# Kernel tuning notes

Hardware: AMD Instinct MI355X
Metric: run time of the kernel (lower is better)

The kernel has to match this reference:

```python
import jax, jax.numpy as jnp
from jax import lax
import numpy as np

EPS = 1e-12  # matches torch F.normalize eps


def _dtw_similarity(s1, s2):
    # s1: [L1, D], s2: [L2, D]
    L1, L2 = s1.shape[0], s2.shape[0]
    s1n = s1 / jnp.maximum(jnp.linalg.norm(s1, axis=1, keepdims=True), EPS)
    s2n = s2 / jnp.maximum(jnp.linalg.norm(s2, axis=1, keepdims=True), EPS)
    dist = 1.0 - s1n @ s2n.T  # [L1, L2] cosine distance

    # DTW DP. Row 0 is a cumsum; each subsequent row has a left-to-right
    # sequential dependency handled by an inner scan.
    row0 = jnp.cumsum(dist[0])

    def row_step(prev_row, d_row):
        # prev_row: dtw[i-1, :], d_row: dist[i, :]
        first = prev_row[0] + d_row[0]  # dtw[i, 0]
        # min(prev[j], prev[j-1]) for j >= 1 (vectorized part of the min)
        p = jnp.minimum(prev_row[1:], prev_row[:-1])

        def col_step(c, inp):
            dj, pj = inp
            new = dj + jnp.minimum(pj, c)  # c = dtw[i, j-1]
            return new, new

        _, rest = lax.scan(col_step, first, (d_row[1:], p))
        new_row = jnp.concatenate([first[None], rest])
        return new_row, None

    last_row, _ = lax.scan(row_step, row0, dist[1:])
    dtw_distance = last_row[-1]
    normalized = dtw_distance / (L1 + L2)
    return 1.0 / (1.0 + normalized)


def setup_inputs() -> dict:
    key = jax.random.key(0)
    k1, k2 = jax.random.split(key)
    seq1 = jax.random.normal(k1, (16, 1024, 768), dtype=jnp.float32)
    seq2 = jax.random.normal(k2, (16, 1024, 768), dtype=jnp.float32)
    return {"seq1": seq1, "seq2": seq2}


def reference(seq1, seq2):
    # seq1: [B, L1, D], seq2: [B, L2, D] -> [B]
    return jax.vmap(_dtw_similarity)(seq1, seq2)
```

## Files before the change

kernel.cpp:

```cpp
#include <hip/hip_runtime.h>
#include <hip/hip_bf16.h>

typedef __attribute__((ext_vector_type(4))) float f32x4;
typedef __attribute__((ext_vector_type(8))) short bf16x8;

#define DINF 1e30f

__device__ __forceinline__ unsigned short f2bf(float f) {
    unsigned int u = __builtin_bit_cast(unsigned int, f);
    u += 0x7FFFu + ((u >> 16) & 1u);
    return (unsigned short)(u >> 16);
}

__global__ __launch_bounds__(256) void zero_holes_kernel(float4* __restrict__ skew) {
    const int idx = blockIdx.x;
    const int bt  = idx / 127;
    const int pr  = idx % 127;
    const int h   = pr * 2 + (threadIdx.x >> 7);
    const int row = h < 126 ? h : 1024 + (h - 126);
    const int c   = threadIdx.x & 127;
    skew[((size_t)bt * 1152 + row) * 128 + c] = (float4){0.f, 0.f, 0.f, 0.f};
}

__global__ __launch_bounds__(256) void norm_bf16_kernel(
    const float* __restrict__ s1, const float* __restrict__ s2,
    __hip_bfloat16* __restrict__ o1, __hip_bfloat16* __restrict__ o2) {
    const int gb = blockIdx.x;
    const float* in;
    __hip_bfloat16* out;
    int rowbase;
    if (gb < 4096) { in = s1; out = o1; rowbase = gb * 4; }
    else           { in = s2; out = o2; rowbase = (gb - 4096) * 4; }
    const int wv = threadIdx.x >> 6;
    const int l  = threadIdx.x & 63;
    const int row = rowbase + wv;

    const float* rp = in + (size_t)row * 768 + l * 4;
    float4 x0 = *(const float4*)(rp);
    float4 x1 = *(const float4*)(rp + 256);
    float4 x2 = *(const float4*)(rp + 512);

    float s = x0.x*x0.x + x0.y*x0.y + x0.z*x0.z + x0.w*x0.w
            + x1.x*x1.x + x1.y*x1.y + x1.z*x1.z + x1.w*x1.w
            + x2.x*x2.x + x2.y*x2.y + x2.z*x2.z + x2.w*x2.w;
#pragma unroll
    for (int off = 32; off > 0; off >>= 1) s += __shfl_xor(s, off, 64);

    const float inv = 1.0f / fmaxf(sqrtf(s), 1e-12f);

    __hip_bfloat16* op = out + (size_t)row * 768 + l * 4;
    ushort4 o;
    o.x = f2bf(x0.x*inv); o.y = f2bf(x0.y*inv); o.z = f2bf(x0.z*inv); o.w = f2bf(x0.w*inv);
    *(ushort4*)(op) = o;
    o.x = f2bf(x1.x*inv); o.y = f2bf(x1.y*inv); o.z = f2bf(x1.z*inv); o.w = f2bf(x1.w*inv);
    *(ushort4*)(op + 256) = o;
    o.x = f2bf(x2.x*inv); o.y = f2bf(x2.y*inv); o.z = f2bf(x2.z*inv); o.w = f2bf(x2.w*inv);
    *(ushort4*)(op + 512) = o;
}

#define GLOAD_LDS16(g, l)                                                      \
    __builtin_amdgcn_global_load_lds(                                          \
        (const __attribute__((address_space(1))) void*)(g),                    \
        (__attribute__((address_space(3))) void*)(l), 16, 0, 0)

__global__ __launch_bounds__(256) void gemm_dist_kernel(
    const __hip_bfloat16* __restrict__ A, const __hip_bfloat16* __restrict__ B,
    __hip_bfloat16* __restrict__ skew) {
    __shared__ __hip_bfloat16 lA[128 * 64];
    __shared__ __hip_bfloat16 lB[128 * 64];

    const int blk  = (blockIdx.x & 7) * 128 + (blockIdx.x >> 3);
    const int b    = blk >> 6;
    const int tile = blk & 63;
    const int tm = tile >> 3, tn = tile & 7;
    const int tid  = threadIdx.x;
    const int lane = tid & 63, w = tid >> 6;
    const int lr = lane & 15, lg = lane >> 4;
    const int wm = w >> 1, wn = w & 1;

    const __hip_bfloat16* Ab = A + (size_t)b * (1024 * 768) + (size_t)(tm * 128) * 768;
    const __hip_bfloat16* Bb = B + (size_t)b * (1024 * 768) + (size_t)(tn * 128) * 768;

    const int srow = tid >> 3;
    const int scol = (tid & 7) * 8;

    char* lAb = (char*)lA;
    char* lBb = (char*)lB;

    f32x4 acc[4][4];
#pragma unroll
    for (int m = 0; m < 4; ++m)
#pragma unroll
        for (int n = 0; n < 4; ++n) acc[m][n] = (f32x4){0.f, 0.f, 0.f, 0.f};

    for (int k0 = 0; k0 < 768; k0 += 64) {
#pragma unroll
        for (int q = 0; q < 4; ++q) {
            GLOAD_LDS16(Ab + (size_t)(q * 32 + srow) * 768 + k0 + scol,
                        lAb + q * 4096 + w * 1024);
            GLOAD_LDS16(Bb + (size_t)(q * 32 + srow) * 768 + k0 + scol,
                        lBb + q * 4096 + w * 1024);
        }
        __syncthreads();

#pragma unroll
        for (int ks = 0; ks < 64; ks += 32) {
            bf16x8 af[4], bfr[4];
#pragma unroll
            for (int m = 0; m < 4; ++m)
                af[m] = *(const bf16x8*)&lA[(wm * 64 + m * 16 + lr) * 64 + ks + lg * 8];
#pragma unroll
            for (int n = 0; n < 4; ++n)
                bfr[n] = *(const bf16x8*)&lB[(wn * 64 + n * 16 + lr) * 64 + ks + lg * 8];
#pragma unroll
            for (int m = 0; m < 4; ++m)
#pragma unroll
                for (int n = 0; n < 4; ++n)
                    acc[m][n] = __builtin_amdgcn_mfma_f32_16x16x32_bf16(af[m], bfr[n], acc[m][n], 0, 0, 0);
        }
        __syncthreads();
    }

    unsigned short* S = (unsigned short*)skew + (size_t)b * (1152 * 1024);
#pragma unroll
    for (int m = 0; m < 4; ++m)
#pragma unroll
        for (int n = 0; n < 4; ++n) {
            const int cb = tn * 128 + wn * 64 + n * 16;
            const int soff = 2 * (cb >> 4);
#pragma unroll
            for (int r = 0; r < 4; ++r) {
                const int row = tm * 128 + wm * 64 + m * 16 + lg * 4 + r;
                S[(size_t)(row + soff) * 1024 + cb + lr] = f2bf(1.0f - acc[m][n][r]);
            }
        }
}


#define VWAIT(n) asm volatile("s_waitcnt vmcnt(" #n ")" ::: "memory")

#define GLDMA16(g, l)                                                          \
    __builtin_amdgcn_global_load_lds(                                          \
        (const __attribute__((address_space(1))) void*)(g),                    \
        (__attribute__((address_space(3))) void*)(l), 16, 0, 0)

#define LOADR(BK, SL, RW) do {                                                 \
    const char* g_ = Sb + ((size_t)(RW) << 11);                                \
    GLDMA16(g_,      &ring[BK][SL][0][0]);                                     \
    GLDMA16(g_ + 16, &ring[BK][SL][1][0]);                                     \
} while (0)

#define ISSUE8(BK, BASE) do {                                                  \
    LOADR(BK, 0, (BASE));     LOADR(BK, 1, (BASE) + 1);                        \
    LOADR(BK, 2, (BASE) + 2); LOADR(BK, 3, (BASE) + 3);                        \
    LOADR(BK, 4, (BASE) + 4); LOADR(BK, 5, (BASE) + 5);                        \
    LOADR(BK, 6, (BASE) + 6); LOADR(BK, 7, (BASE) + 7);                        \
} while (0)

#define DECLR(N) float4 N##_0, N##_1

#define DSRD(BK, SL, N) do {                                                   \
    N##_0 = ring[BK][SL][0][t]; N##_1 = ring[BK][SL][1][t];                    \
} while (0)

#define DSRD8(BK) do {                                                         \
    DSRD(BK, 0, R0); DSRD(BK, 1, R1); DSRD(BK, 2, R2); DSRD(BK, 3, R3);        \
    DSRD(BK, 4, R4); DSRD(BK, 5, R5); DSRD(BK, 6, R6); DSRD(BK, 7, R7);        \
} while (0)

#define STEPBODY(P, E0EXPR) do {                                               \
    unsigned u0_ = __builtin_bit_cast(unsigned, P##_0.x);                      \
    unsigned u1_ = __builtin_bit_cast(unsigned, P##_0.y);                      \
    unsigned u2_ = __builtin_bit_cast(unsigned, P##_0.z);                      \
    unsigned u3_ = __builtin_bit_cast(unsigned, P##_0.w);                      \
    unsigned u4_ = __builtin_bit_cast(unsigned, P##_1.x);                      \
    unsigned u5_ = __builtin_bit_cast(unsigned, P##_1.y);                      \
    unsigned u6_ = __builtin_bit_cast(unsigned, P##_1.z);                      \
    unsigned u7_ = __builtin_bit_cast(unsigned, P##_1.w);                      \
    float d0_  = __builtin_bit_cast(float, u0_ << 16);                         \
    float d1_  = __builtin_bit_cast(float, u0_ & 0xffff0000u);                 \
    float d2_  = __builtin_bit_cast(float, u1_ << 16);                         \
    float d3_  = __builtin_bit_cast(float, u1_ & 0xffff0000u);                 \
    float d4_  = __builtin_bit_cast(float, u2_ << 16);                         \
    float d5_  = __builtin_bit_cast(float, u2_ & 0xffff0000u);                 \
    float d6_  = __builtin_bit_cast(float, u3_ << 16);                         \
    float d7_  = __builtin_bit_cast(float, u3_ & 0xffff0000u);                 \
    float d8_  = __builtin_bit_cast(float, u4_ << 16);                         \
    float d9_  = __builtin_bit_cast(float, u4_ & 0xffff0000u);                 \
    float d10_ = __builtin_bit_cast(float, u5_ << 16);                         \
    float d11_ = __builtin_bit_cast(float, u5_ & 0xffff0000u);                 \
    float d12_ = __builtin_bit_cast(float, u6_ << 16);                         \
    float d13_ = __builtin_bit_cast(float, u6_ & 0xffff0000u);                 \
    float d14_ = __builtin_bit_cast(float, u7_ << 16);                         \
    float d15_ = __builtin_bit_cast(float, u7_ & 0xffff0000u);                 \
    float e0_ = (E0EXPR);                                                      \
    float c0_  = d0_  + e0_;                                                   \
    float c1_  = d1_  + fminf(fminf(p1,  p0),  c0_);                           \
    float c2_  = d2_  + fminf(fminf(p2,  p1),  c1_);                           \
    float c3_  = d3_  + fminf(fminf(p3,  p2),  c2_);                           \
    float c4_  = d4_  + fminf(fminf(p4,  p3),  c3_);                           \
    float c5_  = d5_  + fminf(fminf(p5,  p4),  c4_);                           \
    float c6_  = d6_  + fminf(fminf(p6,  p5),  c5_);                           \
    float c7_  = d7_  + fminf(fminf(p7,  p6),  c6_);                           \
    float c8_  = d8_  + fminf(fminf(p8,  p7),  c7_);                           \
    float c9_  = d9_  + fminf(fminf(p9,  p8),  c8_);                           \
    float c10_ = d10_ + fminf(fminf(p10, p9),  c9_);                           \
    float c11_ = d11_ + fminf(fminf(p11, p10), c10_);                          \
    float c12_ = d12_ + fminf(fminf(p12, p11), c11_);                          \
    float c13_ = d13_ + fminf(fminf(p13, p12), c12_);                          \
    float c14_ = d14_ + fminf(fminf(p14, p13), c13_);                          \
    float c15_ = d15_ + fminf(fminf(p15, p14), c14_);                          \
    p0=c0_; p1=c1_; p2=c2_; p3=c3_; p4=c4_; p5=c5_; p6=c6_; p7=c7_;            \
    p8=c8_; p9=c9_; p10=c10_; p11=c11_; p12=c12_; p13=c13_; p14=c14_; p15=c15_;\
    a3 = a2; a2 = a1;                                                          \
    a1 = __shfl_up(c15_, 1, 64);                                               \
    a1 = lane0 ? DINF : a1;                                                    \
} while (0)

#define STEPB(P)       STEPBODY(P, fminf(fminf(p0, a3), a2))
#define STEPB_FIRST(P) STEPBODY(P, lane0 ? 0.0f : fminf(fminf(p0, a3), a2))

#define STEP8() do {                                                           \
    STEPB(R0); STEPB(R1); STEPB(R2); STEPB(R3);                                \
    STEPB(R4); STEPB(R5); STEPB(R6); STEPB(R7);                                \
} while (0)

__global__ __launch_bounds__(64, 1) void dtw_dp_kernel(
    const __hip_bfloat16* __restrict__ skew, float* __restrict__ out) {
    __shared__ float4 ring[3][8][2][64];

    const int b = blockIdx.x;
    const int t = threadIdx.x;
    const bool lane0 = (t == 0);
    const char* Sb = (const char*)(skew + (size_t)b * (1152 * 1024)) + (t << 5);

    float p0 = DINF, p1 = DINF, p2 = DINF, p3 = DINF,
          p4 = DINF, p5 = DINF, p6 = DINF, p7 = DINF,
          p8 = DINF, p9 = DINF, p10 = DINF, p11 = DINF,
          p12 = DINF, p13 = DINF, p14 = DINF, p15 = DINF;
    float a1 = DINF, a2 = DINF, a3 = DINF;

    DECLR(R0); DECLR(R1); DECLR(R2); DECLR(R3);
    DECLR(R4); DECLR(R5); DECLR(R6); DECLR(R7);

    ISSUE8(0, 0);
    ISSUE8(1, 8);

    ISSUE8(2, 16);
    VWAIT(16);
    DSRD8(0);
    STEPB_FIRST(R0);
    STEPB(R1); STEPB(R2); STEPB(R3); STEPB(R4); STEPB(R5); STEPB(R6); STEPB(R7);

    int rb = 1, ib = 0, base = 24;
#pragma unroll 1
    for (int j = 1; j < 142; ++j) {
        ISSUE8(ib, base);
        VWAIT(16);
        DSRD8(rb);
        STEP8();
        rb = rb == 2 ? 0 : rb + 1;
        ib = ib == 2 ? 0 : ib + 1;
        base += 8;
    }

    VWAIT(8);
    DSRD8(1);
    STEP8();
    VWAIT(0);
    DSRD(2, 0, R0); DSRD(2, 1, R1); DSRD(2, 2, R2);
    DSRD(2, 3, R3); DSRD(2, 4, R4); DSRD(2, 5, R5);
    STEPB(R0); STEPB(R1); STEPB(R2); STEPB(R3); STEPB(R4); STEPB(R5);

    if (t == 63) out[b] = 1.0f / (1.0f + p15 * (1.0f / 2048.0f));
}

extern "C" void kernel_launch(void* const* d_in, const int* in_sizes, int n_in,
                              void* d_out, int out_size, void* d_ws, size_t ws_size,
                              hipStream_t stream) {
    const float* s1 = (const float*)d_in[0];
    const float* s2 = (const float*)d_in[1];
    float* out = (float*)d_out;

    char* ws = (char*)d_ws;
    __hip_bfloat16* Abf  = (__hip_bfloat16*)(ws);
    __hip_bfloat16* Bbf  = (__hip_bfloat16*)(ws + 25165824);
    __hip_bfloat16* skew = (__hip_bfloat16*)(ws + 50331648);

    zero_holes_kernel<<<16 * 127, 256, 0, stream>>>((float4*)skew);
    norm_bf16_kernel<<<8192, 256, 0, stream>>>(s1, s2, Abf, Bbf);
    gemm_dist_kernel<<<16 * 64, 256, 0, stream>>>(Abf, Bbf, skew);
    dtw_dp_kernel<<<16, 64, 0, stream>>>(skew, out);
}
```

Before: 260.8 us.

## Interleave two batch DTW chains per wavefront and pipeline LDS reads

```diff
diff --git a/kernel.cpp b/kernel.cpp
--- a/kernel.cpp
+++ b/kernel.cpp
@@ -144,135 +144,179 @@
         (const __attribute__((address_space(1))) void*)(g),                    \
         (__attribute__((address_space(3))) void*)(l), 16, 0, 0)
 
-#define LOADR(BK, SL, RW) do {                                                 \
-    const char* g_ = Sb + ((size_t)(RW) << 11);                                \
-    GLDMA16(g_,      &ring[BK][SL][0][0]);                                     \
-    GLDMA16(g_ + 16, &ring[BK][SL][1][0]);                                     \
+#define LOADR(BAT, BK, SL, RW) do {                                            \
+    const char* g_ = Sb##BAT + ((size_t)(RW) << 11);                           \
+    GLDMA16(g_,      &ring[BAT][BK][SL][0][0]);                                \
+    GLDMA16(g_ + 16, &ring[BAT][BK][SL][1][0]);                                \
 } while (0)
 
-#define ISSUE8(BK, BASE) do {                                                  \
-    LOADR(BK, 0, (BASE));     LOADR(BK, 1, (BASE) + 1);                        \
-    LOADR(BK, 2, (BASE) + 2); LOADR(BK, 3, (BASE) + 3);                        \
-    LOADR(BK, 4, (BASE) + 4); LOADR(BK, 5, (BASE) + 5);                        \
-    LOADR(BK, 6, (BASE) + 6); LOADR(BK, 7, (BASE) + 7);                        \
+#define ISSUE16(BK, BASE) do {                                                 \
+    LOADR(0, BK, 0, (BASE));     LOADR(1, BK, 0, (BASE));                      \
+    LOADR(0, BK, 1, (BASE) + 1); LOADR(1, BK, 1, (BASE) + 1);                  \
+    LOADR(0, BK, 2, (BASE) + 2); LOADR(1, BK, 2, (BASE) + 2);                  \
+    LOADR(0, BK, 3, (BASE) + 3); LOADR(1, BK, 3, (BASE) + 3);                  \
+    LOADR(0, BK, 4, (BASE) + 4); LOADR(1, BK, 4, (BASE) + 4);                  \
+    LOADR(0, BK, 5, (BASE) + 5); LOADR(1, BK, 5, (BASE) + 5);                  \
+    LOADR(0, BK, 6, (BASE) + 6); LOADR(1, BK, 6, (BASE) + 6);                  \
+    LOADR(0, BK, 7, (BASE) + 7); LOADR(1, BK, 7, (BASE) + 7);                  \
 } while (0)
 
-#define DECLR(N) float4 N##_0, N##_1
-
-#define DSRD(BK, SL, N) do {                                                   \
-    N##_0 = ring[BK][SL][0][t]; N##_1 = ring[BK][SL][1][t];                    \
+#define DSRD2(BK, SL, PA, PB) do {                                             \
+    PA##_0 = ring[0][BK][SL][0][t]; PB##_0 = ring[1][BK][SL][0][t];            \
+    PA##_1 = ring[0][BK][SL][1][t]; PB##_1 = ring[1][BK][SL][1][t];            \
 } while (0)
 
-#define DSRD8(BK) do {                                                         \
-    DSRD(BK, 0, R0); DSRD(BK, 1, R1); DSRD(BK, 2, R2); DSRD(BK, 3, R3);        \
-    DSRD(BK, 4, R4); DSRD(BK, 5, R5); DSRD(BK, 6, R6); DSRD(BK, 7, R7);        \
+#define BFLO(u) __builtin_bit_cast(float, (unsigned)((u) << 16))
+#define BFHI(u) __builtin_bit_cast(float, (unsigned)((u) & 0xffff0000u))
+
+#define STEPDUO(PA, PB, E0A, E0B) do {                                         \
+    unsigned uA0_ = __builtin_bit_cast(unsigned, PA##_0.x);                    \
+    unsigned uB0_ = __builtin_bit_cast(unsigned, PB##_0.x);                    \
+    unsigned uA1_ = __builtin_bit_cast(unsigned, PA##_0.y);                    \
+    unsigned uB1_ = __builtin_bit_cast(unsigned, PB##_0.y);                    \
+    unsigned uA2_ = __builtin_bit_cast(unsigned, PA##_0.z);                    \
+    unsigned uB2_ = __builtin_bit_cast(unsigned, PB##_0.z);                    \
+    unsigned uA3_ = __builtin_bit_cast(unsigned, PA##_0.w);                    \
+    unsigned uB3_ = __builtin_bit_cast(unsigned, PB##_0.w);                    \
+    unsigned uA4_ = __builtin_bit_cast(unsigned, PA##_1.x);                    \
+    unsigned uB4_ = __builtin_bit_cast(unsigned, PB##_1.x);                    \
+    unsigned uA5_ = __builtin_bit_cast(unsigned, PA##_1.y);                    \
+    unsigned uB5_ = __builtin_bit_cast(unsigned, PB##_1.y);                    \
+    unsigned uA6_ = __builtin_bit_cast(unsigned, PA##_1.z);                    \
+    unsigned uB6_ = __builtin_bit_cast(unsigned, PB##_1.z);                    \
+    unsigned uA7_ = __builtin_bit_cast(unsigned, PA##_1.w);                    \
+    unsigned uB7_ = __builtin_bit_cast(unsigned, PB##_1.w);                    \
+    float eA_ = (E0A);                  float eB_ = (E0B);                     \
+    float cA0_  = BFLO(uA0_) + eA_;                                            \
+    float cB0_  = BFLO(uB0_) + eB_;                                            \
+    float cA1_  = BFHI(uA0_) + fminf(fminf(pA1,  pA0),  cA0_);                 \
+    float cB1_  = BFHI(uB0_) + fminf(fminf(pB1,  pB0),  cB0_);                 \
+    float cA2_  = BFLO(uA1_) + fminf(fminf(pA2,  pA1),  cA1_);                 \
+    float cB2_  = BFLO(uB1_) + fminf(fminf(pB2,  pB1),  cB1_);                 \
+    float cA3_  = BFHI(uA1_) + fminf(fminf(pA3,  pA2),  cA2_);                 \
+    float cB3_  = BFHI(uB1_) + fminf(fminf(pB3,  pB2),  cB2_);                 \
+    float cA4_  = BFLO(uA2_) + fminf(fminf(pA4,  pA3),  cA3_);                 \
+    float cB4_  = BFLO(uB2_) + fminf(fminf(pB4,  pB3),  cB3_);                 \
+    float cA5_  = BFHI(uA2_) + fminf(fminf(pA5,  pA4),  cA4_);                 \
+    float cB5_  = BFHI(uB2_) + fminf(fminf(pB5,  pB4),  cB4_);                 \
+    float cA6_  = BFLO(uA3_) + fminf(fminf(pA6,  pA5),  cA5_);                 \
+    float cB6_  = BFLO(uB3_) + fminf(fminf(pB6,  pB5),  cB5_);                 \
+    float cA7_  = BFHI(uA3_) + fminf(fminf(pA7,  pA6),  cA6_);                 \
+    float cB7_  = BFHI(uB3_) + fminf(fminf(pB7,  pB6),  cB6_);                 \
+    float cA8_  = BFLO(uA4_) + fminf(fminf(pA8,  pA7),  cA7_);                 \
+    float cB8_  = BFLO(uB4_) + fminf(fminf(pB8,  pB7),  cB7_);                 \
+    float cA9_  = BFHI(uA4_) + fminf(fminf(pA9,  pA8),  cA8_);                 \
+    float cB9_  = BFHI(uB4_) + fminf(fminf(pB9,  pB8),  cB8_);                 \
+    float cA10_ = BFLO(uA5_) + fminf(fminf(pA10, pA9),  cA9_);                 \
+    float cB10_ = BFLO(uB5_) + fminf(fminf(pB10, pB9),  cB9_);                 \
+    float cA11_ = BFHI(uA5_) + fminf(fminf(pA11, pA10), cA10_);                \
+    float cB11_ = BFHI(uB5_) + fminf(fminf(pB11, pB10), cB10_);                \
+    float cA12_ = BFLO(uA6_) + fminf(fminf(pA12, pA11), cA11_);                \
+    float cB12_ = BFLO(uB6_) + fminf(fminf(pB12, pB11), cB11_);                \
+    float cA13_ = BFHI(uA6_) + fminf(fminf(pA13, pA12), cA12_);                \
+    float cB13_ = BFHI(uB6_) + fminf(fminf(pB13, pB12), cB12_);                \
+    float cA14_ = BFLO(uA7_) + fminf(fminf(pA14, pA13), cA13_);                \
+    float cB14_ = BFLO(uB7_) + fminf(fminf(pB14, pB13), cB13_);                \
+    float cA15_ = BFHI(uA7_) + fminf(fminf(pA15, pA14), cA14_);                \
+    float cB15_ = BFHI(uB7_) + fminf(fminf(pB15, pB14), cB14_);                \
+    pA0=cA0_; pA1=cA1_; pA2=cA2_; pA3=cA3_; pA4=cA4_; pA5=cA5_; pA6=cA6_;      \
+    pA7=cA7_; pA8=cA8_; pA9=cA9_; pA10=cA10_; pA11=cA11_; pA12=cA12_;          \
+    pA13=cA13_; pA14=cA14_; pA15=cA15_;                                        \
+    pB0=cB0_; pB1=cB1_; pB2=cB2_; pB3=cB3_; pB4=cB4_; pB5=cB5_; pB6=cB6_;      \
+    pB7=cB7_; pB8=cB8_; pB9=cB9_; pB10=cB10_; pB11=cB11_; pB12=cB12_;          \
+    pB13=cB13_; pB14=cB14_; pB15=cB15_;                                        \
+    a3A = a2A; a2A = a1A;                                                      \
+    a3B = a2B; a2B = a1B;                                                      \
+    a1A = __shfl_up(cA15_, 1, 64);                                             \
+    a1B = __shfl_up(cB15_, 1, 64);                                             \
+    a1A = lane0 ? DINF : a1A;                                                  \
+    a1B = lane0 ? DINF : a1B;                                                  \
 } while (0)
 
-#define STEPBODY(P, E0EXPR) do {                                               \
-    unsigned u0_ = __builtin_bit_cast(unsigned, P##_0.x);                      \
-    unsigned u1_ = __builtin_bit_cast(unsigned, P##_0.y);                      \
-    unsigned u2_ = __builtin_bit_cast(unsigned, P##_0.z);                      \
-    unsigned u3_ = __builtin_bit_cast(unsigned, P##_0.w);                      \
-    unsigned u4_ = __builtin_bit_cast(unsigned, P##_1.x);                      \
-    unsigned u5_ = __builtin_bit_cast(unsigned, P##_1.y);                      \
-    unsigned u6_ = __builtin_bit_cast(unsigned, P##_1.z);                      \
-    unsigned u7_ = __builtin_bit_cast(unsigned, P##_1.w);                      \
-    float d0_  = __builtin_bit_cast(float, u0_ << 16);                         \
-    float d1_  = __builtin_bit_cast(float, u0_ & 0xffff0000u);                 \
-    float d2_  = __builtin_bit_cast(float, u1_ << 16);                         \
-    float d3_  = __builtin_bit_cast(float, u1_ & 0xffff0000u);                 \
-    float d4_  = __builtin_bit_cast(float, u2_ << 16);                         \
-    float d5_  = __builtin_bit_cast(float, u2_ & 0xffff0000u);                 \
-    float d6_  = __builtin_bit_cast(float, u3_ << 16);                         \
-    float d7_  = __builtin_bit_cast(float, u3_ & 0xffff0000u);                 \
-    float d8_  = __builtin_bit_cast(float, u4_ << 16);                         \
-    float d9_  = __builtin_bit_cast(float, u4_ & 0xffff0000u);                 \
-    float d10_ = __builtin_bit_cast(float, u5_ << 16);                         \
-    float d11_ = __builtin_bit_cast(float, u5_ & 0xffff0000u);                 \
-    float d12_ = __builtin_bit_cast(float, u6_ << 16);                         \
-    float d13_ = __builtin_bit_cast(float, u6_ & 0xffff0000u);                 \
-    float d14_ = __builtin_bit_cast(float, u7_ << 16);                         \
-    float d15_ = __builtin_bit_cast(float, u7_ & 0xffff0000u);                 \
-    float e0_ = (E0EXPR);                                                      \
-    float c0_  = d0_  + e0_;                                                   \
-    float c1_  = d1_  + fminf(fminf(p1,  p0),  c0_);                           \
-    float c2_  = d2_  + fminf(fminf(p2,  p1),  c1_);                           \
-    float c3_  = d3_  + fminf(fminf(p3,  p2),  c2_);                           \
-    float c4_  = d4_  + fminf(fminf(p4,  p3),  c3_);                           \
-    float c5_  = d5_  + fminf(fminf(p5,  p4),  c4_);                           \
-    float c6_  = d6_  + fminf(fminf(p6,  p5),  c5_);                           \
-    float c7_  = d7_  + fminf(fminf(p7,  p6),  c6_);                           \
-    float c8_  = d8_  + fminf(fminf(p8,  p7),  c7_);                           \
-    float c9_  = d9_  + fminf(fminf(p9,  p8),  c8_);                           \
-    float c10_ = d10_ + fminf(fminf(p10, p9),  c9_);                           \
-    float c11_ = d11_ + fminf(fminf(p11, p10), c10_);                          \
-    float c12_ = d12_ + fminf(fminf(p12, p11), c11_);                          \
-    float c13_ = d13_ + fminf(fminf(p13, p12), c12_);                          \
-    float c14_ = d14_ + fminf(fminf(p14, p13), c13_);                          \
-    float c15_ = d15_ + fminf(fminf(p15, p14), c14_);                          \
-    p0=c0_; p1=c1_; p2=c2_; p3=c3_; p4=c4_; p5=c5_; p6=c6_; p7=c7_;            \
-    p8=c8_; p9=c9_; p10=c10_; p11=c11_; p12=c12_; p13=c13_; p14=c14_; p15=c15_;\
-    a3 = a2; a2 = a1;                                                          \
-    a1 = __shfl_up(c15_, 1, 64);                                               \
-    a1 = lane0 ? DINF : a1;                                                    \
-} while (0)
-
-#define STEPB(P)       STEPBODY(P, fminf(fminf(p0, a3), a2))
-#define STEPB_FIRST(P) STEPBODY(P, lane0 ? 0.0f : fminf(fminf(p0, a3), a2))
-
-#define STEP8() do {                                                           \
-    STEPB(R0); STEPB(R1); STEPB(R2); STEPB(R3);                                \
-    STEPB(R4); STEPB(R5); STEPB(R6); STEPB(R7);                                \
-} while (0)
+#define E0A_ fminf(fminf(pA0, a3A), a2A)
+#define E0B_ fminf(fminf(pB0, a3B), a2B)
+#define STEP2(PA, PB)       STEPDUO(PA, PB, E0A_, E0B_)
+#define STEP2_FIRST(PA, PB) STEPDUO(PA, PB, lane0 ? 0.0f : E0A_, lane0 ? 0.0f : E0B_)
 
 __global__ __launch_bounds__(64, 1) void dtw_dp_kernel(
     const __hip_bfloat16* __restrict__ skew, float* __restrict__ out) {
-    __shared__ float4 ring[3][8][2][64];
-
-    const int b = blockIdx.x;
-    const int t = threadIdx.x;
+    __shared__ float4 ring[2][2][8][2][64];
+
+    const int b0 = blockIdx.x * 2;
+    const int t  = threadIdx.x;
     const bool lane0 = (t == 0);
-    const char* Sb = (const char*)(skew + (size_t)b * (1152 * 1024)) + (t << 5);
-
-    float p0 = DINF, p1 = DINF, p2 = DINF, p3 = DINF,
-          p4 = DINF, p5 = DINF, p6 = DINF, p7 = DINF,
-          p8 = DINF, p9 = DINF, p10 = DINF, p11 = DINF,
-          p12 = DINF, p13 = DINF, p14 = DINF, p15 = DINF;
-    float a1 = DINF, a2 = DINF, a3 = DINF;
-
-    DECLR(R0); DECLR(R1); DECLR(R2); DECLR(R3);
-    DECLR(R4); DECLR(R5); DECLR(R6); DECLR(R7);
-
-    ISSUE8(0, 0);
-    ISSUE8(1, 8);
-
-    ISSUE8(2, 16);
-    VWAIT(16);
-    DSRD8(0);
-    STEPB_FIRST(R0);
-    STEPB(R1); STEPB(R2); STEPB(R3); STEPB(R4); STEPB(R5); STEPB(R6); STEPB(R7);
-
-    int rb = 1, ib = 0, base = 24;
+    const char* Sb0 = (const char*)skew + (size_t)b0 * 2359296 + (t << 5);
+    const char* Sb1 = Sb0 + 2359296;
+
+    float pA0 = DINF, pA1 = DINF, pA2 = DINF, pA3 = DINF,
+          pA4 = DINF, pA5 = DINF, pA6 = DINF, pA7 = DINF,
+          pA8 = DINF, pA9 = DINF, pA10 = DINF, pA11 = DINF,
+          pA12 = DINF, pA13 = DINF, pA14 = DINF, pA15 = DINF;
+    float pB0 = DINF, pB1 = DINF, pB2 = DINF, pB3 = DINF,
+          pB4 = DINF, pB5 = DINF, pB6 = DINF, pB7 = DINF,
+          pB8 = DINF, pB9 = DINF, pB10 = DINF, pB11 = DINF,
+          pB12 = DINF, pB13 = DINF, pB14 = DINF, pB15 = DINF;
+    float a1A = DINF, a2A = DINF, a3A = DINF;
+    float a1B = DINF, a2B = DINF, a3B = DINF;
+
+    float4 XA_0, XA_1, XB_0, XB_1;
+    float4 YA_0, YA_1, YB_0, YB_1;
+
+    ISSUE16(0, 0);
+    ISSUE16(1, 8);
+    VWAIT(32);
+    DSRD2(0, 0, XA, XB); DSRD2(0, 1, YA, YB);
+
+    STEP2_FIRST(XA, XB); DSRD2(0, 2, XA, XB);
+    STEP2(YA, YB);       DSRD2(0, 3, YA, YB);
+    STEP2(XA, XB);       DSRD2(0, 4, XA, XB);
+    STEP2(YA, YB);       DSRD2(0, 5, YA, YB);
+    STEP2(XA, XB);       DSRD2(0, 6, XA, XB);
+    STEP2(YA, YB);       DSRD2(0, 7, YA, YB);
+    VWAIT(0);
+    STEP2(XA, XB);       DSRD2(1, 0, XA, XB);
+    STEP2(YA, YB);       DSRD2(1, 1, YA, YB);
+    ISSUE16(0, 16);
+
+    int rb = 1, base = 24;
 #pragma unroll 1
     for (int j = 1; j < 142; ++j) {
-        ISSUE8(ib, base);
-        VWAIT(16);
-        DSRD8(rb);
-        STEP8();
-        rb = rb == 2 ? 0 : rb + 1;
-        ib = ib == 2 ? 0 : ib + 1;
+        const int nb = rb ^ 1;
+        STEP2(XA, XB); DSRD2(rb, 2, XA, XB);
+        STEP2(YA, YB); DSRD2(rb, 3, YA, YB);
+        STEP2(XA, XB); DSRD2(rb, 4, XA, XB);
+        STEP2(YA, YB); DSRD2(rb, 5, YA, YB);
+        STEP2(XA, XB); DSRD2(rb, 6, XA, XB);
+        STEP2(YA, YB); DSRD2(rb, 7, YA, YB);
+        VWAIT(0);
+        STEP2(XA, XB); DSRD2(nb, 0, XA, XB);
+        STEP2(YA, YB); DSRD2(nb, 1, YA, YB);
+        ISSUE16(rb, base);
+        rb = nb;
         base += 8;
     }
 
-    VWAIT(8);
-    DSRD8(1);
-    STEP8();
+    STEP2(XA, XB); DSRD2(0, 2, XA, XB);
+    STEP2(YA, YB); DSRD2(0, 3, YA, YB);
+    STEP2(XA, XB); DSRD2(0, 4, XA, XB);
+    STEP2(YA, YB); DSRD2(0, 5, YA, YB);
+    STEP2(XA, XB); DSRD2(0, 6, XA, XB);
+    STEP2(YA, YB); DSRD2(0, 7, YA, YB);
     VWAIT(0);
-    DSRD(2, 0, R0); DSRD(2, 1, R1); DSRD(2, 2, R2);
-    DSRD(2, 3, R3); DSRD(2, 4, R4); DSRD(2, 5, R5);
-    STEPB(R0); STEPB(R1); STEPB(R2); STEPB(R3); STEPB(R4); STEPB(R5);
-
-    if (t == 63) out[b] = 1.0f / (1.0f + p15 * (1.0f / 2048.0f));
+    STEP2(XA, XB); DSRD2(1, 0, XA, XB);
+    STEP2(YA, YB); DSRD2(1, 1, YA, YB);
+
+    STEP2(XA, XB); DSRD2(1, 2, XA, XB);
+    STEP2(YA, YB); DSRD2(1, 3, YA, YB);
+    STEP2(XA, XB); DSRD2(1, 4, XA, XB);
+    STEP2(YA, YB); DSRD2(1, 5, YA, YB);
+    STEP2(XA, XB);
+    STEP2(YA, YB);
+
+    if (t == 63) {
+        out[b0]     = 1.0f / (1.0f + pA15 * (1.0f / 2048.0f));
+        out[b0 + 1] = 1.0f / (1.0f + pB15 * (1.0f / 2048.0f));
+    }
 }
 
 extern "C" void kernel_launch(void* const* d_in, const int* in_sizes, int n_in,
@@ -290,5 +334,5 @@
     zero_holes_kernel<<<16 * 127, 256, 0, stream>>>((float4*)skew);
     norm_bf16_kernel<<<8192, 256, 0, stream>>>(s1, s2, Abf, Bbf);
     gemm_dist_kernel<<<16 * 64, 256, 0, stream>>>(Abf, Bbf, skew);
-    dtw_dp_kernel<<<16, 64, 0, stream>>>(skew, out);
-}
+    dtw_dp_kernel<<<8, 64, 0, stream>>>(skew, out);
+}
```

Result: slower. 345.8 us (+32.6%).
